# Kernel optimization log

Hardware: AMD Instinct MI355X
Metric: run time of the kernel (lower is better)

The kernel has to match this reference:

```python
import jax, jax.numpy as jnp
import numpy as np

EPS = 1.1920929e-07  # torch RMSNorm default eps = finfo(float32).eps

def rmsnorm(x, w):
    return x * jax.lax.rsqrt(jnp.mean(x * x, axis=-1, keepdims=True) + EPS) * w

def setup_inputs() -> dict:
    key = jax.random.key(0)
    ks = jax.random.split(key, 12)
    D, H, SC, ST = 1024, 16, 64, 16
    B, T = 2, 2048
    s = 0.02
    return {
        "x": jax.random.normal(ks[0], (B, T, D), jnp.float32),
        "qkv_w": jax.random.normal(ks[1], (3 * D, D), jnp.float32) * s,
        "o_w": jax.random.normal(ks[2], (D, D), jnp.float32) * s,
        "norm1_w": jnp.ones((D,), jnp.float32),
        "norm2_w": jnp.ones((D,), jnp.float32),
        "in_w": jax.random.normal(ks[3], (SC, D), jnp.float32) * s,
        "out_w": jax.random.normal(ks[4], (D, SC), jnp.float32) * s,  # zeros in torch init; randn for nontrivial baseline
        "A_log": jax.random.normal(ks[5], (SC, ST), jnp.float32) * 0.1,
        "Bp_w": jax.random.normal(ks[6], (ST, SC), jnp.float32) * s,
        "Cp_w": jax.random.normal(ks[7], (ST, SC), jnp.float32) * s,
        "dt_w": jax.random.normal(ks[8], (SC, SC), jnp.float32) * s,
        "dt_b": jnp.full((SC,), -3.0, jnp.float32),
        "gate_w": jax.random.normal(ks[9], (SC, D), jnp.float32) * s,
    }

def selective_scan(h, in_w, out_w, A_log, Bp_w, Cp_w, dt_w, dt_b, gate_w):
    B, T, D = h.shape
    SC, ST = A_log.shape
    z = h @ in_w.T                      # [B,T,SC]
    gate = jax.nn.silu(h @ gate_w.T)    # [B,T,SC]
    A = -jnp.exp(A_log)                 # [SC,ST]
    Bi = z @ Bp_w.T                     # [B,T,ST]
    Ci = z @ Cp_w.T                     # [B,T,ST]
    dt = jax.nn.softplus(z @ dt_w.T + dt_b)  # [B,T,SC]
    A_bar = 1.0 + dt[..., None] * A     # [B,T,SC,ST]

    def step(state, inp):
        a_bar, dtz_t, b_t, c_t = inp    # [B,SC,ST],[B,SC],[B,ST],[B,ST]
        state = a_bar * state + dtz_t[:, :, None] * b_t[:, None, :]
        y = jnp.sum(state * c_t[:, None, :], axis=-1)  # [B,SC]
        return state, y

    init = jnp.zeros((B, SC, ST), h.dtype)
    xs = (jnp.swapaxes(A_bar, 0, 1), jnp.swapaxes(dt * z, 0, 1),
          jnp.swapaxes(Bi, 0, 1), jnp.swapaxes(Ci, 0, 1))
    _, ys = jax.lax.scan(step, init, xs)      # [T,B,SC]
    y = jnp.swapaxes(ys, 0, 1) * gate         # [B,T,SC]
    return y @ out_w.T                        # [B,T,D]

def reference(x, qkv_w, o_w, norm1_w, norm2_w, in_w, out_w, A_log, Bp_w, Cp_w, dt_w, dt_b, gate_w):
    B, T, D = x.shape
    H = 16
    hd = D // H
    h = rmsnorm(x, norm1_w)
    qkv = (h @ qkv_w.T).reshape(B, T, 3, H, hd)
    qkv = jnp.transpose(qkv, (2, 0, 3, 1, 4))  # [3,B,H,T,hd]
    q, k, v = qkv[0], qkv[1], qkv[2]
    attn = jnp.einsum('bhqd,bhkd->bhqk', q, k) / np.sqrt(hd).astype(np.float32)
    mask = jnp.tril(jnp.ones((T, T), bool))
    attn = jnp.where(mask, attn, -jnp.inf)
    attn = jax.nn.softmax(attn, axis=-1)
    out = jnp.einsum('bhqk,bhkd->bhqd', attn, v)
    out = jnp.transpose(out, (0, 2, 1, 3)).reshape(B, T, D)
    x = x + out @ o_w.T
    h2 = rmsnorm(x, norm2_w)
    x = x + selective_scan(h2, in_w, out_w, A_log, Bp_w, Cp_w, dt_w, dt_b, gate_w)
    return x
```

## Files before the change

kernel.cpp:

```cpp
#include <hip/hip_runtime.h>
#include <hip/hip_bf16.h>
#include <math.h>

typedef __hip_bfloat16 bf16;
typedef __attribute__((ext_vector_type(4))) float v_f32x4;
typedef __attribute__((ext_vector_type(4))) unsigned short v_u16x4;
typedef __attribute__((ext_vector_type(8))) unsigned short v_u16x8;
typedef __attribute__((ext_vector_type(8))) __bf16 v_bf16x8;

#define NB 2
#define NT 2048
#define ND 1024
#define NH 16
#define NSC 64
#define NST 16
#define NM (NB*NT)
#define RMS_EPS 1.1920929e-07f
#define NCHUNK 32
#define CLEN 64

__device__ inline float b2f(unsigned short u) {
  union { unsigned int i; float f; } v; v.i = ((unsigned int)u) << 16; return v.f;
}
__device__ inline unsigned short f2b(float f) {
  union { float f; unsigned int i; } v; v.f = f;
  unsigned int r = (v.i + 0x7FFF + ((v.i >> 16) & 1)) >> 16;
  return (unsigned short)r;
}

__device__ inline void gl_lds16(const bf16* g, bf16* l) {
  __builtin_amdgcn_global_load_lds((__attribute__((address_space(1))) void*)g,
                                   (__attribute__((address_space(3))) void*)l,
                                   16, 0, 0);
}

__global__ __launch_bounds__(256) void cvt_rms_kernel(
    const float* __restrict__ qkv_w, const float* __restrict__ o_w,
    const float* __restrict__ out_w, const float* __restrict__ in_w,
    const float* __restrict__ gate_w, const float* __restrict__ dt_w,
    const float* __restrict__ Bp_w, const float* __restrict__ Cp_w,
    bf16* __restrict__ qkvw_b, bf16* __restrict__ ow_b, bf16* __restrict__ outw_b,
    bf16* __restrict__ W1, bf16* __restrict__ W2,
    const float* __restrict__ x, const float* __restrict__ n1w, bf16* __restrict__ h) {
  const int blk = blockIdx.x, t = threadIdx.x;
  if (blk >= 4295) {
    const int row = blk - 4295;
    v_f32x4 xv = *(const v_f32x4*)(x + (size_t)row * ND + t * 4);
    float s = xv[0]*xv[0] + xv[1]*xv[1] + xv[2]*xv[2] + xv[3]*xv[3];
    #pragma unroll
    for (int off = 32; off; off >>= 1) s += __shfl_xor(s, off, 64);
    __shared__ float red[4];
    __shared__ float scale_s;
    if ((t & 63) == 0) red[t >> 6] = s;
    __syncthreads();
    if (t == 0) scale_s = rsqrtf((red[0] + red[1] + red[2] + red[3]) * (1.0f / ND) + RMS_EPS);
    __syncthreads();
    float sc = scale_s;
    v_f32x4 wv = *(const v_f32x4*)(n1w + t * 4);
    v_u16x4 o;
    o[0] = f2b(xv[0] * sc * wv[0]);
    o[1] = f2b(xv[1] * sc * wv[1]);
    o[2] = f2b(xv[2] * sc * wv[2]);
    o[3] = f2b(xv[3] * sc * wv[3]);
    *(v_u16x4*)((unsigned short*)h + (size_t)row * ND + t * 4) = o;
    return;
  }
  const float* src; bf16* dst; int base;
  if (blk < 3072)      { src = qkv_w;  dst = qkvw_b;      base = blk; }
  else if (blk < 4096) { src = o_w;    dst = ow_b;        base = blk - 3072; }
  else if (blk < 4160) { src = out_w;  dst = outw_b;      base = blk - 4096; }
  else if (blk < 4224) { src = in_w;   dst = W1;          base = blk - 4160; }
  else if (blk < 4288) { src = gate_w; dst = W1 + 65536;  base = blk - 4224; }
  else if (blk < 4292) { src = dt_w;   dst = W2;          base = blk - 4288; }
  else if (blk == 4292){ src = Bp_w;   dst = W2 + 4096;   base = 0; }
  else if (blk == 4293){ src = Cp_w;   dst = W2 + 5120;   base = 0; }
  else {
    v_u16x8 z;
    #pragma unroll
    for (int i = 0; i < 8; i++) z[i] = 0;
    *(v_u16x8*)(W2 + 6144 + t * 8) = z;
    return;
  }
  int i = base * 256 + t;
  v_f32x4 v = ((const v_f32x4*)src)[i];
  v_u16x4 o;
  o[0] = f2b(v[0]); o[1] = f2b(v[1]); o[2] = f2b(v[2]); o[3] = f2b(v[3]);
  ((v_u16x4*)dst)[i] = o;
}

template <bool RES, bool OUTF32>
__global__ __launch_bounds__(256) void gemm_bt_kernel(
    const bf16* __restrict__ A, const bf16* __restrict__ Bw,
    const float* __restrict__ res, void* __restrict__ Cout, int N, int K, int lda) {
  __shared__ alignas(16) bf16 As[128 * 32];
  __shared__ alignas(16) bf16 Bs[128 * 32];
  const int tid = threadIdx.x;
  const int wid = tid >> 6;
  const int lane = tid & 63;
  const int c = lane & 15;
  const int quad = lane >> 4;
  const int m0 = blockIdx.y * 128;
  const int n0 = blockIdx.x * 128;
  const int wm = (wid >> 1) * 64;
  const int wn = (wid & 1) * 64;
  const int srow = tid >> 2;
  const int schunk = tid & 3;

  const bf16* Ap0 = A + (size_t)(m0 + srow) * lda + schunk * 8;
  const bf16* Ap1 = Ap0 + (size_t)64 * lda;
  const bf16* Bp0 = Bw + (size_t)(n0 + srow) * K + schunk * 8;
  const bf16* Bp1 = Bp0 + (size_t)64 * K;
  bf16* AsW0 = As + wid * 512;
  bf16* AsW1 = As + 2048 + wid * 512;
  bf16* BsW0 = Bs + wid * 512;
  bf16* BsW1 = Bs + 2048 + wid * 512;

  v_f32x4 acc[4][4];
  #pragma unroll
  for (int i = 0; i < 4; i++)
    #pragma unroll
    for (int j = 0; j < 4; j++)
      #pragma unroll
      for (int r = 0; r < 4; r++) acc[i][j][r] = 0.0f;

  const int nk = K >> 5;
  for (int kt = 0; kt < nk; kt++) {
    gl_lds16(Ap0 + kt * 32, AsW0);
    gl_lds16(Ap1 + kt * 32, AsW1);
    gl_lds16(Bp0 + kt * 32, BsW0);
    gl_lds16(Bp1 + kt * 32, BsW1);
    __syncthreads();
    v_bf16x8 af[4], bfw[4];
    #pragma unroll
    for (int i = 0; i < 4; i++)
      af[i] = *(const v_bf16x8*)&As[(wm + i * 16 + c) * 32 + quad * 8];
    #pragma unroll
    for (int j = 0; j < 4; j++)
      bfw[j] = *(const v_bf16x8*)&Bs[(wn + j * 16 + c) * 32 + quad * 8];
    #pragma unroll
    for (int i = 0; i < 4; i++)
      #pragma unroll
      for (int j = 0; j < 4; j++)
        acc[i][j] = __builtin_amdgcn_mfma_f32_16x16x32_bf16(af[i], bfw[j], acc[i][j], 0, 0, 0);
    __syncthreads();
  }

  #pragma unroll
  for (int i = 0; i < 4; i++)
    #pragma unroll
    for (int j = 0; j < 4; j++)
      #pragma unroll
      for (int r = 0; r < 4; r++) {
        int rg = m0 + wm + i * 16 + quad * 4 + r;
        int cg = n0 + wn + j * 16 + c;
        size_t idx = (size_t)rg * N + cg;
        float v = acc[i][j][r];
        if (RES) v += res[idx];
        if (OUTF32) ((float*)Cout)[idx] = v;
        else ((bf16*)Cout)[idx] = __float2bfloat16(v);
      }
}

template <bool RES, bool OUTF32>
__global__ __launch_bounds__(256) void gemm_bt64_kernel(
    const bf16* __restrict__ A, const bf16* __restrict__ Bw,
    const float* __restrict__ res, void* __restrict__ Cout, int N, int K, int lda) {
  __shared__ alignas(16) bf16 As[64 * 32];
  __shared__ alignas(16) bf16 Bs[128 * 32];
  const int tid = threadIdx.x;
  const int wid = tid >> 6;
  const int lane = tid & 63;
  const int c = lane & 15;
  const int quad = lane >> 4;
  const int m0 = blockIdx.y * 64;
  const int n0 = blockIdx.x * 128;
  const int wm = (wid & 1) * 32;
  const int wn = (wid >> 1) * 64;
  const int srow = tid >> 2;
  const int schunk = tid & 3;

  const bf16* Ap = A + (size_t)(m0 + srow) * lda + schunk * 8;
  const bf16* Bp0 = Bw + (size_t)(n0 + srow) * K + schunk * 8;
  const bf16* Bp1 = Bp0 + (size_t)64 * K;
  bf16* AsW  = As + wid * 512;
  bf16* BsW0 = Bs + wid * 512;
  bf16* BsW1 = Bs + 2048 + wid * 512;

  v_f32x4 acc[2][4];
  #pragma unroll
  for (int i = 0; i < 2; i++)
    #pragma unroll
    for (int j = 0; j < 4; j++)
      #pragma unroll
      for (int r = 0; r < 4; r++) acc[i][j][r] = 0.0f;

  const int nk = K >> 5;
  for (int kt = 0; kt < nk; kt++) {
    gl_lds16(Ap + kt * 32, AsW);
    gl_lds16(Bp0 + kt * 32, BsW0);
    gl_lds16(Bp1 + kt * 32, BsW1);
    __syncthreads();
    v_bf16x8 af[2], bfw[4];
    #pragma unroll
    for (int i = 0; i < 2; i++)
      af[i] = *(const v_bf16x8*)&As[(wm + i * 16 + c) * 32 + quad * 8];
    #pragma unroll
    for (int j = 0; j < 4; j++)
      bfw[j] = *(const v_bf16x8*)&Bs[(wn + j * 16 + c) * 32 + quad * 8];
    #pragma unroll
    for (int i = 0; i < 2; i++)
      #pragma unroll
      for (int j = 0; j < 4; j++)
        acc[i][j] = __builtin_amdgcn_mfma_f32_16x16x32_bf16(af[i], bfw[j], acc[i][j], 0, 0, 0);
    __syncthreads();
  }

  #pragma unroll
  for (int i = 0; i < 2; i++)
    #pragma unroll
    for (int j = 0; j < 4; j++)
      #pragma unroll
      for (int r = 0; r < 4; r++) {
        int rg = m0 + wm + i * 16 + quad * 4 + r;
        int cg = n0 + wn + j * 16 + c;
        size_t idx = (size_t)rg * N + cg;
        float v = acc[i][j][r];
        if (RES) v += res[idx];
        if (OUTF32) ((float*)Cout)[idx] = v;
        else ((bf16*)Cout)[idx] = __float2bfloat16(v);
      }
}

__global__ __launch_bounds__(256) void vtrans_kernel(const bf16* __restrict__ qkv,
                                                     bf16* __restrict__ VtG) {
  __shared__ alignas(16) bf16 Vs[64 * 72];
  const int tid = threadIdx.x;
  const int t0 = blockIdx.x * 64;
  const int bh = blockIdx.y;
  const int b = bh >> 4, h = bh & 15;
  const int srow = tid >> 2, schunk = tid & 3;
  {
    const bf16* src = qkv + (size_t)(b * NT + t0 + srow) * 3072 + 2048 + h * 64 + schunk * 16;
    *(v_u16x8*)&Vs[srow * 72 + schunk * 16] = *(const v_u16x8*)src;
    *(v_u16x8*)&Vs[srow * 72 + schunk * 16 + 8] = *(const v_u16x8*)(src + 8);
  }
  __syncthreads();
  const unsigned short* Vsu = (const unsigned short*)Vs;
  v_u16x8 a, bvec;
  #pragma unroll
  for (int i = 0; i < 8; i++) a[i] = Vsu[(schunk * 16 + i) * 72 + srow];
  #pragma unroll
  for (int i = 0; i < 8; i++) bvec[i] = Vsu[(schunk * 16 + 8 + i) * 72 + srow];
  bf16* dst = VtG + (size_t)(bh * 64 + srow) * NT + t0 + schunk * 16;
  *(v_u16x8*)dst = a;
  *(v_u16x8*)(dst + 8) = bvec;
}

__global__ __launch_bounds__(256) void attn_kernel(const bf16* __restrict__ qkv,
                                                   const bf16* __restrict__ VtG,
                                                   bf16* __restrict__ out) {
  __shared__ alignas(16) bf16 Qs[64 * 72];
  __shared__ alignas(16) bf16 Ks[64 * 72];
  __shared__ alignas(16) bf16 Vt[64 * 72];
  __shared__ alignas(16) bf16 Ps[64 * 72];
  const int tid = threadIdx.x;
  const int w = tid >> 6;
  const int lane = tid & 63;
  const int c = lane & 15;
  const int quad = lane >> 4;
  const int id = blockIdx.x;
  const int bh = id & 31;
  const int j5 = id >> 5;
  const int j0 = j5 & 7;
  const int qt = (j5 & 24) | (((j5 >> 3) & 1) ? (7 - j0) : j0);
  const int b = bh >> 4;
  const int h = bh & 15;
  const int srow = tid >> 2;
  const int schunk = tid & 3;

  {
    const bf16* src = qkv + (size_t)(b * NT + qt * 64 + srow) * 3072 + h * 64 + schunk * 16;
    *(v_u16x8*)&Qs[srow * 72 + schunk * 16] = *(const v_u16x8*)src;
    *(v_u16x8*)&Qs[srow * 72 + schunk * 16 + 8] = *(const v_u16x8*)(src + 8);
  }
  __syncthreads();
  v_bf16x8 aq0 = *(const v_bf16x8*)&Qs[(w * 16 + c) * 72 + quad * 8];
  v_bf16x8 aq1 = *(const v_bf16x8*)&Qs[(w * 16 + c) * 72 + 32 + quad * 8];

  float l_part[4];
  v_f32x4 o[4];
  #pragma unroll
  for (int r = 0; r < 4; r++) l_part[r] = 0.0f;
  #pragma unroll
  for (int j = 0; j < 4; j++)
    #pragma unroll
    for (int r = 0; r < 4; r++) o[j][r] = 0.0f;

  for (int kt = 0; kt <= qt; kt++) {
    {
      const bf16* ksrc = qkv + (size_t)(b * NT + kt * 64 + srow) * 3072 + 1024 + h * 64 + schunk * 16;
      *(v_u16x8*)&Ks[srow * 72 + schunk * 16] = *(const v_u16x8*)ksrc;
      *(v_u16x8*)&Ks[srow * 72 + schunk * 16 + 8] = *(const v_u16x8*)(ksrc + 8);
      const bf16* vsrc = VtG + (size_t)(bh * 64 + srow) * NT + kt * 64 + schunk * 16;
      *(v_u16x8*)&Vt[srow * 72 + schunk * 16] = *(const v_u16x8*)vsrc;
      *(v_u16x8*)&Vt[srow * 72 + schunk * 16 + 8] = *(const v_u16x8*)(vsrc + 8);
    }
    __syncthreads();

    const bool diag = (kt == qt);
    #pragma unroll
    for (int j = 0; j < 4; j++) {
      v_bf16x8 bk0 = *(const v_bf16x8*)&Ks[(j * 16 + c) * 72 + quad * 8];
      v_bf16x8 bk1 = *(const v_bf16x8*)&Ks[(j * 16 + c) * 72 + 32 + quad * 8];
      v_f32x4 z;
      #pragma unroll
      for (int r = 0; r < 4; r++) z[r] = 0.0f;
      z = __builtin_amdgcn_mfma_f32_16x16x32_bf16(aq0, bk0, z, 0, 0, 0);
      z = __builtin_amdgcn_mfma_f32_16x16x32_bf16(aq1, bk1, z, 0, 0, 0);
      #pragma unroll
      for (int r = 0; r < 4; r++) {
        float p = __expf(z[r] * 0.125f);
        if (diag && (j * 16 + c) > (w * 16 + quad * 4 + r)) p = 0.0f;
        l_part[r] += p;
        Ps[(w * 16 + quad * 4 + r) * 72 + j * 16 + c] = __float2bfloat16(p);
      }
    }
    #pragma unroll
    for (int ks = 0; ks < 2; ks++) {
      v_bf16x8 ap = *(const v_bf16x8*)&Ps[(w * 16 + c) * 72 + ks * 32 + quad * 8];
      #pragma unroll
      for (int jn = 0; jn < 4; jn++) {
        v_bf16x8 bv = *(const v_bf16x8*)&Vt[(jn * 16 + c) * 72 + ks * 32 + quad * 8];
        o[jn] = __builtin_amdgcn_mfma_f32_16x16x32_bf16(ap, bv, o[jn], 0, 0, 0);
      }
    }
    __syncthreads();
  }

  #pragma unroll
  for (int r = 0; r < 4; r++) {
    float l = l_part[r];
    l += __shfl_xor(l, 1, 64);
    l += __shfl_xor(l, 2, 64);
    l += __shfl_xor(l, 4, 64);
    l += __shfl_xor(l, 8, 64);
    l_part[r] = l;
  }

  #pragma unroll
  for (int jn = 0; jn < 4; jn++)
    #pragma unroll
    for (int r = 0; r < 4; r++) {
      int qg = qt * 64 + w * 16 + quad * 4 + r;
      out[(size_t)(b * NT + qg) * ND + h * 64 + jn * 16 + c] =
          __float2bfloat16(o[jn][r] / l_part[r]);
    }
}

__global__ __launch_bounds__(256) void proj_scan_kernel(
    const float* __restrict__ x1, const float* __restrict__ n2w,
    const bf16* __restrict__ W1, const bf16* __restrict__ W2,
    const float* __restrict__ dt_b,
    float* __restrict__ dt_a, float* __restrict__ dtz_a,
    float* __restrict__ gate_a, float* __restrict__ P2) {
  __shared__ alignas(16) bf16 h2S[16 * 1032];
  __shared__ alignas(16) bf16 Bs[128 * 32];
  __shared__ alignas(16) bf16 zgS[16 * 136];
  const int tid = threadIdx.x;
  const int w = tid >> 6, lane = tid & 63, c = lane & 15, quad = lane >> 4;
  const int m0 = blockIdx.x * 16;
  unsigned short* h2Su = (unsigned short*)h2S;
  unsigned short* zgSu = (unsigned short*)zgS;

  {
    const int r16 = tid >> 4, ct = tid & 15;
    const float* xr = x1 + (size_t)(m0 + r16) * ND + ct * 64;
    v_f32x4 xv[16];
    float ss = 0.0f;
    #pragma unroll
    for (int i = 0; i < 16; i++) {
      xv[i] = *(const v_f32x4*)(xr + i * 4);
      ss += xv[i][0]*xv[i][0] + xv[i][1]*xv[i][1] + xv[i][2]*xv[i][2] + xv[i][3]*xv[i][3];
    }
    ss += __shfl_xor(ss, 1, 64);
    ss += __shfl_xor(ss, 2, 64);
    ss += __shfl_xor(ss, 4, 64);
    ss += __shfl_xor(ss, 8, 64);
    float sc = rsqrtf(ss * (1.0f / ND) + RMS_EPS);
    const float* wr = n2w + ct * 64;
    #pragma unroll
    for (int i = 0; i < 16; i++) {
      v_f32x4 wv = *(const v_f32x4*)(wr + i * 4);
      v_u16x4 o;
      o[0] = f2b(xv[i][0] * sc * wv[0]);
      o[1] = f2b(xv[i][1] * sc * wv[1]);
      o[2] = f2b(xv[i][2] * sc * wv[2]);
      o[3] = f2b(xv[i][3] * sc * wv[3]);
      *(v_u16x4*)&h2Su[r16 * 1032 + ct * 64 + i * 4] = o;
    }
  }
  __syncthreads();

  const int lrow = lane >> 2, lk = lane & 3;
  v_f32x4 acc[2];
  #pragma unroll
  for (int j = 0; j < 2; j++)
    #pragma unroll
    for (int r = 0; r < 4; r++) acc[j][r] = 0.0f;
  for (int kt = 0; kt < 32; kt++) {
    gl_lds16(W1 + (size_t)(w * 32 + lrow) * 1024 + kt * 32 + lk * 8, Bs + (w * 32) * 32);
    gl_lds16(W1 + (size_t)(w * 32 + 16 + lrow) * 1024 + kt * 32 + lk * 8, Bs + (w * 32 + 16) * 32);
    __syncthreads();
    v_bf16x8 af = *(const v_bf16x8*)&h2S[c * 1032 + kt * 32 + quad * 8];
    #pragma unroll
    for (int j = 0; j < 2; j++) {
      v_bf16x8 bfw = *(const v_bf16x8*)&Bs[(w * 32 + j * 16 + c) * 32 + quad * 8];
      acc[j] = __builtin_amdgcn_mfma_f32_16x16x32_bf16(af, bfw, acc[j], 0, 0, 0);
    }
    __syncthreads();
  }
  #pragma unroll
  for (int j = 0; j < 2; j++)
    #pragma unroll
    for (int r = 0; r < 4; r++)
      zgSu[(quad * 4 + r) * 136 + w * 32 + j * 16 + c] = f2b(acc[j][r]);
  __syncthreads();

  v_f32x4 acc2[2];
  #pragma unroll
  for (int j = 0; j < 2; j++)
    #pragma unroll
    for (int r = 0; r < 4; r++) acc2[j][r] = 0.0f;
  for (int kt = 0; kt < 2; kt++) {
    gl_lds16(W2 + (size_t)(w * 32 + lrow) * 64 + kt * 32 + lk * 8, Bs + (w * 32) * 32);
    gl_lds16(W2 + (size_t)(w * 32 + 16 + lrow) * 64 + kt * 32 + lk * 8, Bs + (w * 32 + 16) * 32);
    __syncthreads();
    v_bf16x8 af = *(const v_bf16x8*)&zgS[c * 136 + kt * 32 + quad * 8];
    #pragma unroll
    for (int j = 0; j < 2; j++) {
      v_bf16x8 bfw = *(const v_bf16x8*)&Bs[(w * 32 + j * 16 + c) * 32 + quad * 8];
      acc2[j] = __builtin_amdgcn_mfma_f32_16x16x32_bf16(af, bfw, acc2[j], 0, 0, 0);
    }
    __syncthreads();
  }

  #pragma unroll
  for (int j = 0; j < 2; j++)
    #pragma unroll
    for (int r = 0; r < 4; r++) {
      const int row = quad * 4 + r;
      const int col = w * 32 + j * 16 + c;
      const size_t grow = (size_t)(m0 + row);
      if (w < 2) {
        float z = b2f(zgSu[row * 136 + col]);
        float a = acc2[j][r] + dt_b[col];
        float dt = (a > 20.0f) ? a : log1pf(__expf(a));
        dt_a[grow * NSC + col] = dt;
        dtz_a[grow * NSC + col] = dt * z;
      } else {
        P2[grow * 128 + col] = acc2[j][r];
        float g = b2f(zgSu[row * 136 + col]);
        gate_a[grow * NSC + (col - 64)] = g / (1.0f + __expf(-g));
      }
    }
}

__global__ __launch_bounds__(256) void scanA_kernel(
    const float* __restrict__ dt_a, const float* __restrict__ dtz_a,
    const float* __restrict__ P2, const float* __restrict__ A_log,
    float* __restrict__ Pbuf, float* __restrict__ Sbuf) {
  __shared__ float dtS[CLEN * 16], dtzS[CLEN * 16], biS[CLEN * 16];
  const int k = blockIdx.x, scg = blockIdx.y, b = blockIdx.z;
  const int tid = threadIdx.x;
  const int t0 = k * CLEN;
  {
    int r = tid >> 2, c4 = (tid & 3) * 4;
    *(v_f32x4*)&dtS[r * 16 + c4]  = *(const v_f32x4*)&dt_a[(size_t)(b * NT + t0 + r) * NSC + scg * 16 + c4];
    *(v_f32x4*)&dtzS[r * 16 + c4] = *(const v_f32x4*)&dtz_a[(size_t)(b * NT + t0 + r) * NSC + scg * 16 + c4];
    *(v_f32x4*)&biS[r * 16 + c4]  = *(const v_f32x4*)&P2[(size_t)(b * NT + t0 + r) * 128 + 64 + c4];
  }
  __syncthreads();
  const int st = tid & 15, scl = tid >> 4;
  const float A = -__expf(A_log[(scg * 16 + scl) * NST + st]);
  float P = 1.0f, s = 0.0f;
  #pragma unroll
  for (int t = 0; t < CLEN; t++) {
    float a = fmaf(dtS[t * 16 + scl], A, 1.0f);
    float u = dtzS[t * 16 + scl] * biS[t * 16 + st];
    P *= a;
    s = fmaf(a, s, u);
  }
  size_t idx = (size_t)(b * NCHUNK + k) * 1024 + scg * 256 + tid;
  Pbuf[idx] = P;
  Sbuf[idx] = s;
}

__global__ __launch_bounds__(256) void scanC_kernel(
    const float* __restrict__ dt_a, const float* __restrict__ dtz_a,
    const float* __restrict__ P2, const float* __restrict__ gate_a,
    const float* __restrict__ A_log, const float* __restrict__ Pbuf,
    const float* __restrict__ Sbuf, bf16* __restrict__ ys) {
  __shared__ float dtS[CLEN * 16], dtzS[CLEN * 16], biS[CLEN * 16], ciS[CLEN * 16], gS[CLEN * 16];
  const int k = blockIdx.x, scg = blockIdx.y, b = blockIdx.z;
  const int tid = threadIdx.x;
  const int t0 = k * CLEN;
  {
    int r = tid >> 2, c4 = (tid & 3) * 4;
    *(v_f32x4*)&dtS[r * 16 + c4]  = *(const v_f32x4*)&dt_a[(size_t)(b * NT + t0 + r) * NSC + scg * 16 + c4];
    *(v_f32x4*)&dtzS[r * 16 + c4] = *(const v_f32x4*)&dtz_a[(size_t)(b * NT + t0 + r) * NSC + scg * 16 + c4];
    *(v_f32x4*)&biS[r * 16 + c4]  = *(const v_f32x4*)&P2[(size_t)(b * NT + t0 + r) * 128 + 64 + c4];
    *(v_f32x4*)&ciS[r * 16 + c4]  = *(const v_f32x4*)&P2[(size_t)(b * NT + t0 + r) * 128 + 80 + c4];
    *(v_f32x4*)&gS[r * 16 + c4]   = *(const v_f32x4*)&gate_a[(size_t)(b * NT + t0 + r) * NSC + scg * 16 + c4];
  }
  const int st = tid & 15, scl = tid >> 4;
  const float A = -__expf(A_log[(scg * 16 + scl) * NST + st]);
  float s = 0.0f;
  for (int kk = 0; kk < k; kk++) {
    size_t idx = (size_t)(b * NCHUNK + kk) * 1024 + scg * 256 + tid;
    s = fmaf(Pbuf[idx], s, Sbuf[idx]);
  }
  __syncthreads();
  for (int t = 0; t < CLEN; t++) {
    float a = fmaf(dtS[t * 16 + scl], A, 1.0f);
    float u = dtzS[t * 16 + scl] * biS[t * 16 + st];
    s = fmaf(a, s, u);
    float pv = s * ciS[t * 16 + st];
    pv += __shfl_xor(pv, 1, 64);
    pv += __shfl_xor(pv, 2, 64);
    pv += __shfl_xor(pv, 4, 64);
    pv += __shfl_xor(pv, 8, 64);
    if (st == 0)
      ys[(size_t)(b * NT + t0 + t) * NSC + scg * 16 + scl] = __float2bfloat16(pv * gS[t * 16 + scl]);
  }
}

extern "C" void kernel_launch(void* const* d_in, const int* in_sizes, int n_in,
                              void* d_out, int out_size, void* d_ws, size_t ws_size,
                              hipStream_t stream) {
  const float* x      = (const float*)d_in[0];
  const float* qkv_w  = (const float*)d_in[1];
  const float* o_w    = (const float*)d_in[2];
  const float* n1w    = (const float*)d_in[3];
  const float* n2w    = (const float*)d_in[4];
  const float* in_w   = (const float*)d_in[5];
  const float* out_w  = (const float*)d_in[6];
  const float* A_log  = (const float*)d_in[7];
  const float* Bp_w   = (const float*)d_in[8];
  const float* Cp_w   = (const float*)d_in[9];
  const float* dt_w   = (const float*)d_in[10];
  const float* dt_b   = (const float*)d_in[11];
  const float* gate_w = (const float*)d_in[12];
  float* out = (float*)d_out;

  char* ws = (char*)d_ws;
  size_t off = 0;
  auto alloc = [&](size_t bytes) {
    char* p = ws + off;
    off += (bytes + 255) & ~(size_t)255;
    return p;
  };
  bf16* qkvw_b = (bf16*)alloc((size_t)3 * ND * ND * 2);
  bf16* ow_b   = (bf16*)alloc((size_t)ND * ND * 2);
  bf16* outw_b = (bf16*)alloc((size_t)ND * NSC * 2);
  bf16* W1     = (bf16*)alloc((size_t)128 * ND * 2);
  bf16* W2     = (bf16*)alloc((size_t)128 * NSC * 2);
  char* region0 = alloc((size_t)NM * 3 * ND * 2);
  char* region1 = alloc((size_t)NM * ND * 2);
  bf16* VtG    = (bf16*)alloc((size_t)NB * NH * 64 * NT * 2);
  float* P2    = (float*)alloc((size_t)NM * 128 * 4);
  float* dt_a  = (float*)alloc((size_t)NM * NSC * 4);
  float* dtz_a = (float*)alloc((size_t)NM * NSC * 4);
  float* gate_a= (float*)alloc((size_t)NM * NSC * 4);
  bf16*  ys    = (bf16*)alloc((size_t)NM * NSC * 2);
  float* Pbuf  = (float*)alloc((size_t)NB * NCHUNK * 1024 * 4);
  float* Sbuf  = (float*)alloc((size_t)NB * NCHUNK * 1024 * 4);

  bf16*  qkv     = (bf16*)region0;
  float* x1      = (float*)region0;
  bf16*  h       = (bf16*)region1;
  bf16*  attnout = (bf16*)region1;

  cvt_rms_kernel<<<4295 + NM, 256, 0, stream>>>(qkv_w, o_w, out_w, in_w, gate_w, dt_w,
                                                Bp_w, Cp_w, qkvw_b, ow_b, outw_b, W1, W2,
                                                x, n1w, h);
  gemm_bt_kernel<false, false><<<dim3(3 * ND / 128, NM / 128), 256, 0, stream>>>(
      h, qkvw_b, nullptr, (void*)qkv, 3 * ND, ND, ND);
  vtrans_kernel<<<dim3(NT / 64, NB * NH), 256, 0, stream>>>(qkv, VtG);
  attn_kernel<<<(NT / 64) * NB * NH, 256, 0, stream>>>(qkv, VtG, attnout);
  gemm_bt64_kernel<true, true><<<dim3(ND / 128, NM / 64), 256, 0, stream>>>(
      attnout, ow_b, x, (void*)x1, ND, ND, ND);
  proj_scan_kernel<<<NM / 16, 256, 0, stream>>>(x1, n2w, W1, W2, dt_b,
                                                dt_a, dtz_a, gate_a, P2);
  scanA_kernel<<<dim3(NCHUNK, 4, NB), 256, 0, stream>>>(dt_a, dtz_a, P2, A_log, Pbuf, Sbuf);
  scanC_kernel<<<dim3(NCHUNK, 4, NB), 256, 0, stream>>>(dt_a, dtz_a, P2, gate_a, A_log,
                                                        Pbuf, Sbuf, ys);
  gemm_bt64_kernel<true, true><<<dim3(ND / 128, NM / 64), 256, 0, stream>>>(
      ys, outw_b, x1, (void*)out, ND, NSC, NSC);
}
```

Baseline: 270.6 us.

## Keep attention probabilities in registers via transposed S computation

The attention kernel now computes S^T (K as the A operand, Q as the B operand), so each lane holds probabilities laid out as a B-operand fragment for a 16x16x16 MFMA. P is fed directly from registers into the PV product instead of going through an LDS buffer. This removes the Ps shared-memory writes and reads and their bank traffic. It also makes the row-sum reduction a two-step shuffle and allows packed vector stores of the output. The cost is twice as many smaller MFMA instructions for PV, plus reading V^T with 8-byte LDS loads.

```diff
diff --git a/kernel.cpp b/kernel.cpp
--- a/kernel.cpp
+++ b/kernel.cpp
@@ -7,6 +7,8 @@
 typedef __attribute__((ext_vector_type(4))) unsigned short v_u16x4;
 typedef __attribute__((ext_vector_type(8))) unsigned short v_u16x8;
 typedef __attribute__((ext_vector_type(8))) __bf16 v_bf16x8;
+typedef __attribute__((ext_vector_type(4))) __bf16 v_bf16x4;
+typedef __attribute__((ext_vector_type(4))) short v_s16x4;
 
 #define NB 2
 #define NT 2048
@@ -26,6 +28,16 @@
   union { float f; unsigned int i; } v; v.f = f;
   unsigned int r = (v.i + 0x7FFF + ((v.i >> 16) & 1)) >> 16;
   return (unsigned short)r;
+}
+
+__device__ inline v_f32x4 mfma16(v_bf16x4 a, v_bf16x4 b, v_f32x4 c) {
+#if __has_builtin(__builtin_amdgcn_mfma_f32_16x16x16_bf16)
+  return __builtin_amdgcn_mfma_f32_16x16x16_bf16(a, b, c, 0, 0, 0);
+#else
+  union U { v_bf16x4 h; v_s16x4 s; };
+  U ua, ub; ua.h = a; ub.h = b;
+  return __builtin_amdgcn_mfma_f32_16x16x16bf16_1k(ua.s, ub.s, c, 0, 0, 0);
+#endif
 }
 
 __device__ inline void gl_lds16(const bf16* g, bf16* l) {
@@ -262,7 +274,6 @@
   __shared__ alignas(16) bf16 Qs[64 * 72];
   __shared__ alignas(16) bf16 Ks[64 * 72];
   __shared__ alignas(16) bf16 Vt[64 * 72];
-  __shared__ alignas(16) bf16 Ps[64 * 72];
   const int tid = threadIdx.x;
   const int w = tid >> 6;
   const int lane = tid & 63;
@@ -287,14 +298,14 @@
   v_bf16x8 aq0 = *(const v_bf16x8*)&Qs[(w * 16 + c) * 72 + quad * 8];
   v_bf16x8 aq1 = *(const v_bf16x8*)&Qs[(w * 16 + c) * 72 + 32 + quad * 8];
 
-  float l_part[4];
+  float l_part = 0.0f;
   v_f32x4 o[4];
   #pragma unroll
-  for (int r = 0; r < 4; r++) l_part[r] = 0.0f;
-  #pragma unroll
-  for (int j = 0; j < 4; j++)
-    #pragma unroll
-    for (int r = 0; r < 4; r++) o[j][r] = 0.0f;
+  for (int jd = 0; jd < 4; jd++)
+    #pragma unroll
+    for (int r = 0; r < 4; r++) o[jd][r] = 0.0f;
+
+  const int qrow = w * 16 + c;
 
   for (int kt = 0; kt <= qt; kt++) {
     {
@@ -308,53 +319,50 @@
     __syncthreads();
 
     const bool diag = (kt == qt);
+    v_bf16x4 pf[4];
     #pragma unroll
     for (int j = 0; j < 4; j++) {
-      v_bf16x8 bk0 = *(const v_bf16x8*)&Ks[(j * 16 + c) * 72 + quad * 8];
-      v_bf16x8 bk1 = *(const v_bf16x8*)&Ks[(j * 16 + c) * 72 + 32 + quad * 8];
+      v_bf16x8 ak0 = *(const v_bf16x8*)&Ks[(j * 16 + c) * 72 + quad * 8];
+      v_bf16x8 ak1 = *(const v_bf16x8*)&Ks[(j * 16 + c) * 72 + 32 + quad * 8];
       v_f32x4 z;
       #pragma unroll
       for (int r = 0; r < 4; r++) z[r] = 0.0f;
-      z = __builtin_amdgcn_mfma_f32_16x16x32_bf16(aq0, bk0, z, 0, 0, 0);
-      z = __builtin_amdgcn_mfma_f32_16x16x32_bf16(aq1, bk1, z, 0, 0, 0);
+      z = __builtin_amdgcn_mfma_f32_16x16x32_bf16(ak0, aq0, z, 0, 0, 0);
+      z = __builtin_amdgcn_mfma_f32_16x16x32_bf16(ak1, aq1, z, 0, 0, 0);
+      v_u16x4 pu;
       #pragma unroll
       for (int r = 0; r < 4; r++) {
         float p = __expf(z[r] * 0.125f);
-        if (diag && (j * 16 + c) > (w * 16 + quad * 4 + r)) p = 0.0f;
-        l_part[r] += p;
-        Ps[(w * 16 + quad * 4 + r) * 72 + j * 16 + c] = __float2bfloat16(p);
+        if (diag && (j * 16 + quad * 4 + r) > qrow) p = 0.0f;
+        l_part += p;
+        pu[r] = f2b(p);
       }
+      union { v_u16x4 u; v_bf16x4 h; } cv; cv.u = pu;
+      pf[j] = cv.h;
     }
     #pragma unroll
-    for (int ks = 0; ks < 2; ks++) {
-      v_bf16x8 ap = *(const v_bf16x8*)&Ps[(w * 16 + c) * 72 + ks * 32 + quad * 8];
-      #pragma unroll
-      for (int jn = 0; jn < 4; jn++) {
-        v_bf16x8 bv = *(const v_bf16x8*)&Vt[(jn * 16 + c) * 72 + ks * 32 + quad * 8];
-        o[jn] = __builtin_amdgcn_mfma_f32_16x16x32_bf16(ap, bv, o[jn], 0, 0, 0);
+    for (int jd = 0; jd < 4; jd++)
+      #pragma unroll
+      for (int j = 0; j < 4; j++) {
+        v_bf16x4 av = *(const v_bf16x4*)&Vt[(jd * 16 + c) * 72 + j * 16 + quad * 4];
+        o[jd] = mfma16(av, pf[j], o[jd]);
       }
-    }
-    __syncthreads();
-  }
-
-  #pragma unroll
-  for (int r = 0; r < 4; r++) {
-    float l = l_part[r];
-    l += __shfl_xor(l, 1, 64);
-    l += __shfl_xor(l, 2, 64);
-    l += __shfl_xor(l, 4, 64);
-    l += __shfl_xor(l, 8, 64);
-    l_part[r] = l;
-  }
-
-  #pragma unroll
-  for (int jn = 0; jn < 4; jn++)
-    #pragma unroll
-    for (int r = 0; r < 4; r++) {
-      int qg = qt * 64 + w * 16 + quad * 4 + r;
-      out[(size_t)(b * NT + qg) * ND + h * 64 + jn * 16 + c] =
-          __float2bfloat16(o[jn][r] / l_part[r]);
-    }
+    __syncthreads();
+  }
+
+  float l = l_part;
+  l += __shfl_xor(l, 16, 64);
+  l += __shfl_xor(l, 32, 64);
+  const float inv = 1.0f / l;
+
+  const int qg = qt * 64 + w * 16 + c;
+  #pragma unroll
+  for (int jd = 0; jd < 4; jd++) {
+    v_u16x4 ov;
+    #pragma unroll
+    for (int r = 0; r < 4; r++) ov[r] = f2b(o[jd][r] * inv);
+    *(v_u16x4*)((unsigned short*)out + (size_t)(b * NT + qg) * ND + h * 64 + jd * 16 + quad * 4) = ov;
+  }
 }
 
 __global__ __launch_bounds__(256) void proj_scan_kernel(
```

New measurement: 269.8 us. About the same (-0.3%).
